# Kernel optimization log

Measured on AMD Instinct MI355X. Metric: run time of the kernel, lower is better.

## Reference

```python
import jax, jax.numpy as jnp
import numpy as np

NBINS = 256
STRENGTH = 100.0
C, H, W = 64, 512, 512


def setup_inputs() -> dict:
    key = jax.random.key(0)
    k1, k2, k3, k4 = jax.random.split(key, 4)
    inp = jax.random.uniform(k1, (1, C, H, W), dtype=jnp.float32)
    tgt = jax.random.uniform(k2, (1, C, H, W), dtype=jnp.float32)
    maskI = jax.random.randint(k3, (1, 1, H, W), 0, 2).astype(jnp.int32)
    maskJ = jax.random.randint(k4, (1, 1, H, W), 0, 2).astype(jnp.int32)
    return {"input": inp, "target": tgt, "maskI": maskI, "maskJ": maskJ}


def _hist_remap(I, J, mI, mJ):
    # I, J: [c, HW] float; mI, mJ: [HW] {0,1} float
    c, hw = I.shape
    nI = mI.sum()
    nJ = mJ.sum()
    big = jnp.float32(1e30)
    # per-channel min/max of masked target values (J[mJ].view(c, nJ).min/max)
    minJ = jnp.min(jnp.where(mJ > 0, J, big), axis=1)   # [c]
    maxJ = jnp.max(jnp.where(mJ > 0, J, -big), axis=1)  # [c]
    step = (maxJ - minJ) / NBINS                          # [c]
    # masked per-channel histogram of target (cu.histogram), scaled by nI/nJ
    binJ = jnp.clip(jnp.floor((J - minJ[:, None]) / jnp.maximum(step[:, None], 1e-12)),
                    0, NBINS - 1).astype(jnp.int32)
    seg = binJ + jnp.arange(c, dtype=jnp.int32)[:, None] * NBINS
    hisJ = jax.ops.segment_sum(jnp.broadcast_to(mJ, (c, hw)).reshape(-1),
                               seg.reshape(-1), num_segments=c * NBINS).reshape(c, NBINS)
    hisJ = hisJ * (nI / nJ)
    cumJ = jnp.cumsum(hisJ, axis=1)                       # [c, nbins]
    # mask input; unmasked pixels -> -1 so they sort to the front (msk_sub trick)
    _I = I * mI - (1.0 - mI)                              # [c, HW]
    idxI = jnp.argsort(_I, axis=1)                        # ascending sort order
    # 1-indexed rank among the nI masked pixels (unmasked ranks <= 0, ignored later)
    rank = jnp.arange(hw, dtype=jnp.float32) - (hw - nI) + 1.0  # [HW]

    def per_ch(cum, his, r, mn, st):
        # CDF inverse: smallest bin b with cum[b] >= rank (cu.hist_remap2)
        b = jnp.clip(jnp.searchsorted(cum, r, side='left'), 0, NBINS - 1)
        lo = cum[b] - his[b]
        ratio = jnp.clip((r - lo) / jnp.maximum(his[b], 1e-12), 0.0, 1.0)
        return mn + (b.astype(jnp.float32) + ratio) * st

    vals = jax.vmap(per_ch)(cumJ, hisJ, jnp.broadcast_to(rank, (c, hw)), minJ, step)  # [c, HW]
    # scatter remapped sorted values back to original pixel positions
    R_sorted = jax.vmap(lambda idx, v: jnp.zeros(hw, dtype=v.dtype).at[idx].set(v))(idxI, vals)
    R = jnp.where(mI > 0, R_sorted, I)
    return R


def reference(input, target, maskI, maskJ):
    _, c, h, w = input.shape
    hw = h * w
    I = input[0].reshape(c, hw)
    J = target[0].reshape(c, hw)
    mI = maskI[0, 0].reshape(hw).astype(jnp.float32)
    mJ = maskJ[0, 0].reshape(hw).astype(jnp.float32)
    R = _hist_remap(I, J, mI, mJ)
    # F.mse_loss(I, R) * strength
    loss = jnp.mean((I - R) ** 2) * STRENGTH
    return loss
```

## Files before the change

### kernel.cpp

```cpp
#include <hip/hip_runtime.h>


#define CN    64
#define HWN   262144
#define NB    256
#define NBUK  8192
#define NBLK  16
#define BPIX  (HWN/NBLK)
#define PT    512
#define XB    64
#define QBUK  (NBUK/4)
#define FXS2  268435456.0f
#define FXSI2 (1.0/268435456.0)

__global__ __launch_bounds__(256) void k_bits(
    const int* __restrict__ mI, const int* __restrict__ mJ,
    unsigned char* __restrict__ bI, unsigned char* __restrict__ bJ)
{
  const int t = blockIdx.x*256 + threadIdx.x;
  const int4* a = (const int4*)mI + 2*t;
  int4 x0 = a[0], x1 = a[1];
  unsigned b = (unsigned)((x0.x>0) | ((x0.y>0)<<1) | ((x0.z>0)<<2) | ((x0.w>0)<<3)
             | ((x1.x>0)<<4) | ((x1.y>0)<<5) | ((x1.z>0)<<6) | ((x1.w>0)<<7));
  const int4* c = (const int4*)mJ + 2*t;
  int4 y0 = c[0], y1 = c[1];
  unsigned d = (unsigned)((y0.x>0) | ((y0.y>0)<<1) | ((y0.z>0)<<2) | ((y0.w>0)<<3)
             | ((y1.x>0)<<4) | ((y1.y>0)<<5) | ((y1.z>0)<<6) | ((y1.w>0)<<7));
  bI[t] = (unsigned char)b;
  bJ[t] = (unsigned char)d;
}

__global__ __launch_bounds__(PT, 4) void k_pass1(
    const float* __restrict__ I, const float* __restrict__ J,
    const unsigned* __restrict__ bI, const unsigned* __restrict__ bJ,
    unsigned* __restrict__ pc, unsigned* __restrict__ qtot,
    unsigned* __restrict__ mnp, unsigned* __restrict__ mxp,
    unsigned* __restrict__ cp, double* __restrict__ qp)
{
  const int c = blockIdx.y, q = blockIdx.x, tid = threadIdx.x;
  const int bid = c*NBLK + q;
  const int wid = tid >> 6, lane = tid & 63;
  __shared__ unsigned buk[NBUK];
  __shared__ unsigned smbI[BPIX/32], smbJ[BPIX/32];
  __shared__ unsigned sred[PT];
  __shared__ double   dred[PT/64];
  __shared__ unsigned umn[PT/64], umx[PT/64], uci[PT/64], ucj[PT/64];
  for(int i = tid; i < NBUK; i += PT) buk[i] = 0u;
  smbI[tid] = bI[q*(BPIX/32) + tid];
  smbJ[tid] = bJ[q*(BPIX/32) + tid];
  __syncthreads();

  const float4* Ic = (const float4*)(I + (size_t)c*HWN + (size_t)q*BPIX);
  const float4* Jc = (const float4*)(J + (size_t)c*HWN + (size_t)q*BPIX);

  float qacc = 0.0f;
  unsigned ci = 0, cj = 0;
  unsigned mn = 0x7F800000u, mx = 0u;
  const int nsh = (tid & 7) * 4;

  float4 pi[2], pj[2];
  pi[0] = Ic[tid]; pj[0] = Jc[tid];
  #pragma unroll
  for(int g = 0; g < 8; g++){
    const int cur = g & 1, nxt = cur ^ 1;
    if(g < 7){ pi[nxt] = Ic[(g+1)*PT + tid]; pj[nxt] = Jc[(g+1)*PT + tid]; }
    const unsigned bitsI = (smbI[g*64 + (tid>>3)] >> nsh) & 0xFu;
    const unsigned bitsJ = (smbJ[g*64 + (tid>>3)] >> nsh) & 0xFu;
    float4 vi4 = pi[cur], vj4 = pj[cur];
    float vv[4] = {vi4.x, vi4.y, vi4.z, vi4.w};
    #pragma unroll
    for(int e = 0; e < 4; e++){
      if(bitsI & (1u << e)){
        float v = vv[e];
        int k = (int)(v * (float)NBUK);
        if(k > NBUK-1) k = NBUK-1;
        float dv = v - ((float)k + 0.5f) * (1.0f/(float)NBUK);
        int fx = (int)rintf(dv * FXS2);
        atomicAdd(&buk[k], ((unsigned)fx << 12) + 1u);
        qacc += dv*dv;
        ci++;
      }
    }
    if(bitsJ & 1u){unsigned u=__float_as_uint(vj4.x); mn=min(mn,u); mx=max(mx,u); cj++;}
    if(bitsJ & 2u){unsigned u=__float_as_uint(vj4.y); mn=min(mn,u); mx=max(mx,u); cj++;}
    if(bitsJ & 4u){unsigned u=__float_as_uint(vj4.z); mn=min(mn,u); mx=max(mx,u); cj++;}
    if(bitsJ & 8u){unsigned u=__float_as_uint(vj4.w); mn=min(mn,u); mx=max(mx,u); cj++;}
  }
  __syncthreads();
  { unsigned* pcb = pc + (size_t)bid * NBUK;
    for(int i = tid; i < NBUK; i += PT) pcb[i] = buk[i]; }

  { unsigned csum = 0;
    #pragma unroll
    for(int j = 0; j < 16; j++) csum += buk[tid*16 + j] & 0xFFFu;
    sred[tid] = csum; __syncthreads();
    for(int s = 64; s > 0; s >>= 1){
      if((tid & 127) < s) sred[tid] += sred[tid + s];
      __syncthreads();
    }
    if((tid & 127) == 0) qtot[bid*4 + (tid >> 7)] = sred[tid];
  }

  double qd = (double)qacc;
  for(int o = 32; o > 0; o >>= 1){
    qd += __shfl_down(qd, o, 64);
    mn  = min(mn, (unsigned)__shfl_down(mn, o, 64));
    mx  = max(mx, (unsigned)__shfl_down(mx, o, 64));
    ci += __shfl_down(ci, o, 64);
    cj += __shfl_down(cj, o, 64);
  }
  if(lane == 0){ dred[wid]=qd; umn[wid]=mn; umx[wid]=mx; uci[wid]=ci; ucj[wid]=cj; }
  __syncthreads();
  if(tid == 0){
    double t = 0.0; unsigned amn=0x7F800000u, amx=0u, aci=0, acj=0;
    for(int w = 0; w < PT/64; w++){
      t += dred[w];
      amn = min(amn, umn[w]); amx = max(amx, umx[w]);
      aci += uci[w]; acj += ucj[w];
    }
    qp[bid] = t;
    mnp[bid] = amn; mxp[bid] = amx;
    if(c == 0){ cp[2*q] = aci; cp[2*q+1] = acj; }
  }
}

__global__ __launch_bounds__(256) void k_histJ(
    const float* __restrict__ J, const unsigned* __restrict__ bJ,
    const unsigned* __restrict__ mnp, const unsigned* __restrict__ mxp,
    unsigned* __restrict__ hisPart, double* __restrict__ lossacc,
    unsigned* __restrict__ donecnt)
{
  const int c = blockIdx.y, xb = blockIdx.x, tid = threadIdx.x;
  if(c == 0 && xb == 0 && tid == 0){ *lossacc = 0.0; *donecnt = 0u; }
  unsigned mnu = 0x7F800000u, mxu = 0u;
  #pragma unroll
  for(int qi = 0; qi < NBLK; qi++){
    mnu = min(mnu, mnp[c*NBLK + qi]);
    mxu = max(mxu, mxp[c*NBLK + qi]);
  }
  float mnv = __uint_as_float(mnu);
  float den = fmaxf((__uint_as_float(mxu) - mnv) / (float)NB, 1e-12f);
  const int SLICE = HWN/XB;
  __shared__ unsigned h[NB];
  __shared__ unsigned smb[SLICE/32];
  h[tid] = 0u;
  if(tid < SLICE/32) smb[tid] = bJ[xb*(SLICE/32) + tid];
  __syncthreads();
  const float4* Jc = (const float4*)(J + (size_t)c*HWN + (size_t)xb*SLICE);
  const int nsh = (tid & 7) * 4;
  #pragma unroll
  for(int it = 0; it < SLICE/1024; ++it){
    int idx = it*256 + tid;
    float4 v4 = Jc[idx];
    const unsigned bits = (smb[it*32 + (tid>>3)] >> nsh) & 0xFu;
    float vv[4] = {v4.x,v4.y,v4.z,v4.w};
    #pragma unroll
    for(int e = 0; e < 4; e++){
      if(bits & (1u << e)){
        float bf = floorf((vv[e] - mnv) / den);
        bf = fminf(fmaxf(bf, 0.0f), 255.0f);
        atomicAdd(&h[(int)bf], 1u);
      }
    }
  }
  __syncthreads();
  hisPart[((size_t)c*XB + xb)*NB + tid] = h[tid];
}

__global__ __launch_bounds__(1024) void k_closs(
    const unsigned* __restrict__ pc, const unsigned* __restrict__ qtot,
    const unsigned* __restrict__ hisPart,
    const unsigned* __restrict__ mnp, const unsigned* __restrict__ mxp,
    const unsigned* __restrict__ cp, const double* __restrict__ qp,
    double* __restrict__ lossacc, unsigned* __restrict__ donecnt,
    float* __restrict__ out)
{
  const int c = blockIdx.x >> 2, qt = blockIdx.x & 3, tid = threadIdx.x;
  const int wid = tid >> 6, lane = tid & 63;
  __shared__ float cs[NB], hs[NB];
  __shared__ unsigned hsum[NB];
  __shared__ unsigned qsh[NBLK*4];
  __shared__ unsigned wsum[16];
  __shared__ double red[16];
  __shared__ float sh_mn, sh_st;
  __shared__ unsigned sh_base;

  if(tid < NB){
    unsigned hr = 0u;
    for(int xb = 0; xb < XB; xb++) hr += hisPart[((size_t)c*XB + xb)*NB + tid];
    hsum[tid] = hr;
  } else if(tid < NB + NBLK*4){
    int k = tid - NB;
    qsh[k] = qtot[(c*NBLK + (k >> 2))*4 + (k & 3)];
  }
  __syncthreads();
  if(tid == 0){
    unsigned ciw = 0, cjw = 0;
    for(int qi = 0; qi < NBLK; qi++){ ciw += cp[2*qi]; cjw += cp[2*qi+1]; }
    float ratio = (float)ciw / (float)cjw;
    float cum = 0.0f;
    for(int b = 0; b < NB; b++){
      float hh = (float)hsum[b] * ratio;
      hs[b] = hh;
      cum += hh;
      cs[b] = cum;
    }
    unsigned mnu = 0x7F800000u, mxu = 0u;
    for(int qi = 0; qi < NBLK; qi++){ mnu = min(mnu, mnp[c*NBLK+qi]); mxu = max(mxu, mxp[c*NBLK+qi]); }
    sh_mn = __uint_as_float(mnu);
    sh_st = (__uint_as_float(mxu) - sh_mn) / (float)NB;
    unsigned base = 0;
    for(int s = 0; s < NBLK; s++)
      for(int q2 = 0; q2 < qt; q2++) base += qsh[s*4 + q2];
    sh_base = base;
  }
  __syncthreads();

  unsigned  kk[2] = {0,0};
  long long ss[2] = {0,0};
  for(int sl = 0; sl < NBLK; sl++){
    const uint2* pcb = (const uint2*)(pc + (size_t)(c*NBLK + sl)*NBUK + qt*QBUK) + tid;
    uint2 w = *pcb;
    kk[0] += w.x & 0xFFFu;  ss[0] += (int)w.x >> 12;
    kk[1] += w.y & 0xFFFu;  ss[1] += (int)w.y >> 12;
  }
  unsigned run = kk[0] + kk[1];
  unsigned v = run;
  for(int o = 1; o < 64; o <<= 1){
    unsigned t = __shfl_up(v, o, 64);
    if(lane >= o) v += t;
  }
  if(lane == 63) wsum[wid] = v;
  __syncthreads();
  unsigned wbase = 0;
  for(int w = 0; w < wid; w++) wbase += wsum[w];
  unsigned texcl = sh_base + wbase + (v - run);

  float  mnvf = sh_mn, stepf = sh_st;
  double mnvd = (double)mnvf, stepd = (double)stepf;

  float rf0 = (float)(texcl + 1u);
  int lo = 0, hi = NB;
  while(lo < hi){ int mid = (lo + hi) >> 1; if(cs[mid] < rf0) lo = mid + 1; else hi = mid; }
  int bin = (lo > NB-1) ? NB-1 : lo;

  double acc = 0.0;
  unsigned r = texcl;
  #pragma unroll
  for(int j = 0; j < 2; j++){
    unsigned k = kk[j];
    if(k == 0) continue;
    unsigned ra = r + 1u, rb = r + k; r = rb;
    double sval = 0.0;
    while(ra <= rb){
      while(bin < NB-1 && cs[bin] < (float)ra) bin++;
      float csb = cs[bin], hsb = hs[bin];
      unsigned re = (bin == NB-1) ? rb : min(rb, (unsigned)floorf(csb));
      double lovd = (double)csb - (double)hsb;
      double den2 = fmax((double)hsb, 1e-12);
      double ra_d = (double)ra, re_d = (double)re, nn = (double)(re - ra + 1u);
      double rta = (ra_d - lovd)/den2, rtb = (re_d - lovd)/den2;
      if(hsb > 0.0f && rta >= 0.0 && rtb <= 1.0){
        double sumr = 0.5*(ra_d + re_d)*nn;
        sval += nn*(mnvd + (double)bin*stepd) + stepd*(sumr - nn*lovd)/den2;
      } else {
        for(unsigned rr = ra; rr <= re; rr++){
          float rf = (float)rr;
          float lov = csb - hsb;
          float rt = (rf - lov) / fmaxf(hsb, 1e-12f);
          rt = fminf(fmaxf(rt, 0.0f), 1.0f);
          sval += (double)(mnvf + ((float)bin + rt)*stepf);
        }
      }
      ra = re + 1u;
    }
    double kb   = (double)k;
    double cb   = ((double)(qt*QBUK + tid*2 + j) + 0.5) * (1.0/(double)NBUK);
    double vbar = sval/kb - cb;
    double S    = (double)ss[j] * FXSI2;
    acc += kb*vbar*vbar - 2.0*vbar*S;
  }
  if(qt == 0 && tid == 0){
    double qsum = 0.0;
    for(int qi = 0; qi < NBLK; qi++) qsum += qp[c*NBLK + qi];
    acc += qsum;
  }
  for(int o = 32; o > 0; o >>= 1) acc += __shfl_down(acc, o, 64);
  if(lane == 0) red[wid] = acc;
  __syncthreads();
  if(tid == 0){
    double t = 0.0;
    for(int w = 0; w < 16; w++) t += red[w];
    atomicAdd(lossacc, t);
    __threadfence();
    unsigned old = atomicAdd(donecnt, 1u);
    if(old == (unsigned)(CN*4 - 1)){
      double tot = atomicAdd(lossacc, 0.0);
      out[0] = (float)(tot * (100.0 / (double)((size_t)CN * HWN)));
    }
  }
}

extern "C" void kernel_launch(void* const* d_in, const int* in_sizes, int n_in,
                              void* d_out, int out_size, void* d_ws, size_t ws_size,
                              hipStream_t stream){
  const float* I  = (const float*)d_in[0];
  const float* J  = (const float*)d_in[1];
  const int*   mI = (const int*)d_in[2];
  const int*   mJ = (const int*)d_in[3];
  float* out = (float*)d_out;

  char* base = (char*)d_ws;
  size_t pcB = (size_t)CN * NBLK * NBUK * sizeof(unsigned);
  size_t hpB = (size_t)CN * XB * NB * sizeof(unsigned);
  size_t qtB = (size_t)CN * NBLK * 4 * sizeof(unsigned);
  unsigned* pc      = (unsigned*)base;
  unsigned* hisPart = (unsigned*)(base + pcB);
  unsigned* qtot    = (unsigned*)(base + pcB + hpB);
  char* p = base + pcB + hpB + qtB;
  double*   qp      = (double*)p;   p += (size_t)CN*NBLK*sizeof(double);
  double*   lossacc = (double*)p;   p += sizeof(double);
  unsigned* mnp     = (unsigned*)p; p += (size_t)CN*NBLK*sizeof(unsigned);
  unsigned* mxp     = (unsigned*)p; p += (size_t)CN*NBLK*sizeof(unsigned);
  unsigned* cp      = (unsigned*)p; p += 2*NBLK*sizeof(unsigned);
  unsigned* donecnt = (unsigned*)p; p += sizeof(unsigned);
  size_t off = (size_t)(p - base); off = (off + 15) & ~(size_t)15;
  unsigned char* bIb = (unsigned char*)(base + off);
  unsigned char* bJb = bIb + HWN/8;

  k_bits<<<HWN/(8*256), 256, 0, stream>>>(mI, mJ, bIb, bJb);
  k_pass1<<<dim3(NBLK, CN), PT, 0, stream>>>(I, J, (const unsigned*)bIb,
                                             (const unsigned*)bJb, pc, qtot,
                                             mnp, mxp, cp, qp);
  k_histJ<<<dim3(XB, CN), 256, 0, stream>>>(J, (const unsigned*)bJb, mnp, mxp,
                                            hisPart, lossacc, donecnt);
  k_closs<<<CN*4, 1024, 0, stream>>>(pc, qtot, hisPart, mnp, mxp, cp, qp,
                                     lossacc, donecnt, out);
}
```

Measured before the change: 189.0 us.

## Front-load all pass1/histJ loads and reshape histJ grid to fewer, larger blocks

k_pass1 now issues all eight float4 loads of I and J, plus the mask words, up front instead of double-buffering them, and its launch bound drops from 4 to 2 blocks per SM to leave room for the extra registers. k_histJ moves from 64 slices of 256 threads to 16 slices of 512 threads, each thread loading all eight vectors at once. Fewer partial histograms are written, and k_closs now spreads the per-bin partial sums across all 1024 threads instead of 256. The goal is more memory-level parallelism and less partial-reduction work, at the cost of higher register pressure and lower occupancy.

```diff
diff --git a/kernel.cpp b/kernel.cpp
--- a/kernel.cpp
+++ b/kernel.cpp
@@ -8,7 +8,8 @@
 #define NBLK  16
 #define BPIX  (HWN/NBLK)
 #define PT    512
-#define XB    64
+#define XB    16
+#define JSL   (HWN/XB)
 #define QBUK  (NBUK/4)
 #define FXS2  268435456.0f
 #define FXSI2 (1.0/268435456.0)
@@ -30,7 +31,31 @@
   bJ[t] = (unsigned char)d;
 }
 
-__global__ __launch_bounds__(PT, 4) void k_pass1(
+__device__ __forceinline__ void px_i(float v, float& qacc, unsigned& ci,
+                                     unsigned* buk){
+  int k = (int)(v * (float)NBUK);
+  if(k > NBUK-1) k = NBUK-1;
+  float dv = v - ((float)k + 0.5f) * (1.0f/(float)NBUK);
+  int fx = (int)rintf(dv * FXS2);
+  atomicAdd(&buk[k], ((unsigned)fx << 12) + 1u);
+  qacc += dv*dv;
+  ci++;
+}
+
+__device__ __forceinline__ void grp_p1(float4 vi4, float4 vj4,
+    unsigned bitsI, unsigned bitsJ, float& qacc, unsigned& ci, unsigned& cj,
+    unsigned& mn, unsigned& mx, unsigned* buk){
+  if(bitsI & 1u) px_i(vi4.x, qacc, ci, buk);
+  if(bitsI & 2u) px_i(vi4.y, qacc, ci, buk);
+  if(bitsI & 4u) px_i(vi4.z, qacc, ci, buk);
+  if(bitsI & 8u) px_i(vi4.w, qacc, ci, buk);
+  if(bitsJ & 1u){unsigned u=__float_as_uint(vj4.x); mn=min(mn,u); mx=max(mx,u); cj++;}
+  if(bitsJ & 2u){unsigned u=__float_as_uint(vj4.y); mn=min(mn,u); mx=max(mx,u); cj++;}
+  if(bitsJ & 4u){unsigned u=__float_as_uint(vj4.z); mn=min(mn,u); mx=max(mx,u); cj++;}
+  if(bitsJ & 8u){unsigned u=__float_as_uint(vj4.w); mn=min(mn,u); mx=max(mx,u); cj++;}
+}
+
+__global__ __launch_bounds__(PT, 2) void k_pass1(
     const float* __restrict__ I, const float* __restrict__ J,
     const unsigned* __restrict__ bI, const unsigned* __restrict__ bJ,
     unsigned* __restrict__ pc, unsigned* __restrict__ qtot,
@@ -57,35 +82,26 @@
   unsigned ci = 0, cj = 0;
   unsigned mn = 0x7F800000u, mx = 0u;
   const int nsh = (tid & 7) * 4;
-
-  float4 pi[2], pj[2];
-  pi[0] = Ic[tid]; pj[0] = Jc[tid];
-  #pragma unroll
-  for(int g = 0; g < 8; g++){
-    const int cur = g & 1, nxt = cur ^ 1;
-    if(g < 7){ pi[nxt] = Ic[(g+1)*PT + tid]; pj[nxt] = Jc[(g+1)*PT + tid]; }
-    const unsigned bitsI = (smbI[g*64 + (tid>>3)] >> nsh) & 0xFu;
-    const unsigned bitsJ = (smbJ[g*64 + (tid>>3)] >> nsh) & 0xFu;
-    float4 vi4 = pi[cur], vj4 = pj[cur];
-    float vv[4] = {vi4.x, vi4.y, vi4.z, vi4.w};
-    #pragma unroll
-    for(int e = 0; e < 4; e++){
-      if(bitsI & (1u << e)){
-        float v = vv[e];
-        int k = (int)(v * (float)NBUK);
-        if(k > NBUK-1) k = NBUK-1;
-        float dv = v - ((float)k + 0.5f) * (1.0f/(float)NBUK);
-        int fx = (int)rintf(dv * FXS2);
-        atomicAdd(&buk[k], ((unsigned)fx << 12) + 1u);
-        qacc += dv*dv;
-        ci++;
-      }
-    }
-    if(bitsJ & 1u){unsigned u=__float_as_uint(vj4.x); mn=min(mn,u); mx=max(mx,u); cj++;}
-    if(bitsJ & 2u){unsigned u=__float_as_uint(vj4.y); mn=min(mn,u); mx=max(mx,u); cj++;}
-    if(bitsJ & 4u){unsigned u=__float_as_uint(vj4.z); mn=min(mn,u); mx=max(mx,u); cj++;}
-    if(bitsJ & 8u){unsigned u=__float_as_uint(vj4.w); mn=min(mn,u); mx=max(mx,u); cj++;}
-  }
+  const int bw  = tid >> 3;
+
+  float4 i0 = Ic[0*PT+tid], i1 = Ic[1*PT+tid], i2 = Ic[2*PT+tid], i3 = Ic[3*PT+tid];
+  float4 i4 = Ic[4*PT+tid], i5 = Ic[5*PT+tid], i6 = Ic[6*PT+tid], i7 = Ic[7*PT+tid];
+  float4 j0 = Jc[0*PT+tid], j1 = Jc[1*PT+tid], j2 = Jc[2*PT+tid], j3 = Jc[3*PT+tid];
+  float4 j4 = Jc[4*PT+tid], j5 = Jc[5*PT+tid], j6 = Jc[6*PT+tid], j7 = Jc[7*PT+tid];
+  unsigned wi0=smbI[0*64+bw], wi1=smbI[1*64+bw], wi2=smbI[2*64+bw], wi3=smbI[3*64+bw];
+  unsigned wi4=smbI[4*64+bw], wi5=smbI[5*64+bw], wi6=smbI[6*64+bw], wi7=smbI[7*64+bw];
+  unsigned wj0=smbJ[0*64+bw], wj1=smbJ[1*64+bw], wj2=smbJ[2*64+bw], wj3=smbJ[3*64+bw];
+  unsigned wj4=smbJ[4*64+bw], wj5=smbJ[5*64+bw], wj6=smbJ[6*64+bw], wj7=smbJ[7*64+bw];
+
+  grp_p1(i0, j0, (wi0>>nsh)&0xFu, (wj0>>nsh)&0xFu, qacc, ci, cj, mn, mx, buk);
+  grp_p1(i1, j1, (wi1>>nsh)&0xFu, (wj1>>nsh)&0xFu, qacc, ci, cj, mn, mx, buk);
+  grp_p1(i2, j2, (wi2>>nsh)&0xFu, (wj2>>nsh)&0xFu, qacc, ci, cj, mn, mx, buk);
+  grp_p1(i3, j3, (wi3>>nsh)&0xFu, (wj3>>nsh)&0xFu, qacc, ci, cj, mn, mx, buk);
+  grp_p1(i4, j4, (wi4>>nsh)&0xFu, (wj4>>nsh)&0xFu, qacc, ci, cj, mn, mx, buk);
+  grp_p1(i5, j5, (wi5>>nsh)&0xFu, (wj5>>nsh)&0xFu, qacc, ci, cj, mn, mx, buk);
+  grp_p1(i6, j6, (wi6>>nsh)&0xFu, (wj6>>nsh)&0xFu, qacc, ci, cj, mn, mx, buk);
+  grp_p1(i7, j7, (wi7>>nsh)&0xFu, (wj7>>nsh)&0xFu, qacc, ci, cj, mn, mx, buk);
+
   __syncthreads();
   { unsigned* pcb = pc + (size_t)bid * NBUK;
     for(int i = tid; i < NBUK; i += PT) pcb[i] = buk[i]; }
@@ -124,7 +140,31 @@
   }
 }
 
-__global__ __launch_bounds__(256) void k_histJ(
+__device__ __forceinline__ void grp_hj(float4 v4, unsigned bits,
+    float mnv, float den, unsigned* h){
+  if(bits & 1u){
+    float bf = floorf((v4.x - mnv) / den);
+    bf = fminf(fmaxf(bf, 0.0f), 255.0f);
+    atomicAdd(&h[(int)bf], 1u);
+  }
+  if(bits & 2u){
+    float bf = floorf((v4.y - mnv) / den);
+    bf = fminf(fmaxf(bf, 0.0f), 255.0f);
+    atomicAdd(&h[(int)bf], 1u);
+  }
+  if(bits & 4u){
+    float bf = floorf((v4.z - mnv) / den);
+    bf = fminf(fmaxf(bf, 0.0f), 255.0f);
+    atomicAdd(&h[(int)bf], 1u);
+  }
+  if(bits & 8u){
+    float bf = floorf((v4.w - mnv) / den);
+    bf = fminf(fmaxf(bf, 0.0f), 255.0f);
+    atomicAdd(&h[(int)bf], 1u);
+  }
+}
+
+__global__ __launch_bounds__(512, 2) void k_histJ(
     const float* __restrict__ J, const unsigned* __restrict__ bJ,
     const unsigned* __restrict__ mnp, const unsigned* __restrict__ mxp,
     unsigned* __restrict__ hisPart, double* __restrict__ lossacc,
@@ -140,31 +180,28 @@
   }
   float mnv = __uint_as_float(mnu);
   float den = fmaxf((__uint_as_float(mxu) - mnv) / (float)NB, 1e-12f);
-  const int SLICE = HWN/XB;
   __shared__ unsigned h[NB];
-  __shared__ unsigned smb[SLICE/32];
-  h[tid] = 0u;
-  if(tid < SLICE/32) smb[tid] = bJ[xb*(SLICE/32) + tid];
-  __syncthreads();
-  const float4* Jc = (const float4*)(J + (size_t)c*HWN + (size_t)xb*SLICE);
+  __shared__ unsigned smb[JSL/32];
+  if(tid < NB) h[tid] = 0u;
+  smb[tid] = bJ[xb*(JSL/32) + tid];
+  __syncthreads();
+  const float4* Jc = (const float4*)(J + (size_t)c*HWN + (size_t)xb*JSL);
   const int nsh = (tid & 7) * 4;
-  #pragma unroll
-  for(int it = 0; it < SLICE/1024; ++it){
-    int idx = it*256 + tid;
-    float4 v4 = Jc[idx];
-    const unsigned bits = (smb[it*32 + (tid>>3)] >> nsh) & 0xFu;
-    float vv[4] = {v4.x,v4.y,v4.z,v4.w};
-    #pragma unroll
-    for(int e = 0; e < 4; e++){
-      if(bits & (1u << e)){
-        float bf = floorf((vv[e] - mnv) / den);
-        bf = fminf(fmaxf(bf, 0.0f), 255.0f);
-        atomicAdd(&h[(int)bf], 1u);
-      }
-    }
-  }
-  __syncthreads();
-  hisPart[((size_t)c*XB + xb)*NB + tid] = h[tid];
+  const int bw  = tid >> 3;
+  float4 v0 = Jc[0*512+tid], v1 = Jc[1*512+tid], v2 = Jc[2*512+tid], v3 = Jc[3*512+tid];
+  float4 v4 = Jc[4*512+tid], v5 = Jc[5*512+tid], v6 = Jc[6*512+tid], v7 = Jc[7*512+tid];
+  unsigned w0=smb[0*64+bw], w1=smb[1*64+bw], w2=smb[2*64+bw], w3=smb[3*64+bw];
+  unsigned w4=smb[4*64+bw], w5=smb[5*64+bw], w6=smb[6*64+bw], w7=smb[7*64+bw];
+  grp_hj(v0, (w0>>nsh)&0xFu, mnv, den, h);
+  grp_hj(v1, (w1>>nsh)&0xFu, mnv, den, h);
+  grp_hj(v2, (w2>>nsh)&0xFu, mnv, den, h);
+  grp_hj(v3, (w3>>nsh)&0xFu, mnv, den, h);
+  grp_hj(v4, (w4>>nsh)&0xFu, mnv, den, h);
+  grp_hj(v5, (w5>>nsh)&0xFu, mnv, den, h);
+  grp_hj(v6, (w6>>nsh)&0xFu, mnv, den, h);
+  grp_hj(v7, (w7>>nsh)&0xFu, mnv, den, h);
+  __syncthreads();
+  if(tid < NB) hisPart[((size_t)c*XB + xb)*NB + tid] = h[tid];
 }
 
 __global__ __launch_bounds__(1024) void k_closs(
@@ -179,20 +216,23 @@
   const int wid = tid >> 6, lane = tid & 63;
   __shared__ float cs[NB], hs[NB];
   __shared__ unsigned hsum[NB];
+  __shared__ unsigned ph[4][NB];
   __shared__ unsigned qsh[NBLK*4];
   __shared__ unsigned wsum[16];
   __shared__ double red[16];
   __shared__ float sh_mn, sh_st;
   __shared__ unsigned sh_base;
 
-  if(tid < NB){
+  { const int part = tid >> 8, bin = tid & 255;
     unsigned hr = 0u;
-    for(int xb = 0; xb < XB; xb++) hr += hisPart[((size_t)c*XB + xb)*NB + tid];
-    hsum[tid] = hr;
-  } else if(tid < NB + NBLK*4){
-    int k = tid - NB;
-    qsh[k] = qtot[(c*NBLK + (k >> 2))*4 + (k & 3)];
-  }
+    #pragma unroll
+    for(int x = 0; x < 4; x++)
+      hr += hisPart[((size_t)c*XB + (part*4 + x))*NB + bin];
+    ph[part][bin] = hr; }
+  if(tid < NBLK*4)
+    qsh[tid] = qtot[(c*NBLK + (tid >> 2))*4 + (tid & 3)];
+  __syncthreads();
+  if(tid < NB) hsum[tid] = ph[0][tid] + ph[1][tid] + ph[2][tid] + ph[3][tid];
   __syncthreads();
   if(tid == 0){
     unsigned ciw = 0, cjw = 0;
@@ -332,7 +372,7 @@
   k_pass1<<<dim3(NBLK, CN), PT, 0, stream>>>(I, J, (const unsigned*)bIb,
                                              (const unsigned*)bJb, pc, qtot,
                                              mnp, mxp, cp, qp);
-  k_histJ<<<dim3(XB, CN), 256, 0, stream>>>(J, (const unsigned*)bJb, mnp, mxp,
+  k_histJ<<<dim3(XB, CN), 512, 0, stream>>>(J, (const unsigned*)bJb, mnp, mxp,
                                             hisPart, lossacc, donecnt);
   k_closs<<<CN*4, 1024, 0, stream>>>(pc, qtot, hisPart, mnp, mxp, cp, qp,
                                      lossacc, donecnt, out);
```

New measurement: 188.1 us. No clear change (-0.5%).

## Fuse pass1, target histogram and loss kernels with per-channel spin barriers

Applied to the files above, without the earlier changes.

Merges the three kernels after the mask-bit pass into one persistent kernel with 4 blocks of 1024 threads per channel. The blocks of a channel meet at global atomic spin barriers before the target histogram and before the loss stage, and the per-block histograms are merged through global atomics. This removes two kernel launches and the separate reread of partial results, and the J slice may still be in cache when the histogram pass reads it. The cost is far fewer blocks (256), which limits parallelism, and the spin barriers assume every block of a channel is resident at the same time.

```diff
diff --git a/kernel.cpp b/kernel.cpp
--- a/kernel.cpp
+++ b/kernel.cpp
@@ -5,19 +5,26 @@
 #define HWN   262144
 #define NB    256
 #define NBUK  8192
-#define NBLK  16
-#define BPIX  (HWN/NBLK)
-#define PT    512
-#define XB    64
+#define NSL   4
+#define QPIX  (HWN/NSL)
+#define FT    1024
 #define QBUK  (NBUK/4)
 #define FXS2  268435456.0f
 #define FXSI2 (1.0/268435456.0)
 
 __global__ __launch_bounds__(256) void k_bits(
     const int* __restrict__ mI, const int* __restrict__ mJ,
-    unsigned char* __restrict__ bI, unsigned char* __restrict__ bJ)
+    unsigned char* __restrict__ bI, unsigned char* __restrict__ bJ,
+    unsigned* __restrict__ ghist, unsigned* __restrict__ syncbuf,
+    double* __restrict__ lossacc, unsigned* __restrict__ donecnt)
 {
   const int t = blockIdx.x*256 + threadIdx.x;
+  if(blockIdx.x < 64){
+    ghist[blockIdx.x*NB + threadIdx.x] = 0u;
+  } else if(blockIdx.x == 64){
+    for(int i = threadIdx.x; i < 2048; i += 256) syncbuf[i] = 0u;
+    if(threadIdx.x == 0){ *lossacc = 0.0; *donecnt = 0u; }
+  }
   const int4* a = (const int4*)mI + 2*t;
   int4 x0 = a[0], x1 = a[1];
   unsigned b = (unsigned)((x0.x>0) | ((x0.y>0)<<1) | ((x0.z>0)<<2) | ((x0.w>0)<<3)
@@ -30,75 +37,91 @@
   bJ[t] = (unsigned char)d;
 }
 
-__global__ __launch_bounds__(PT, 4) void k_pass1(
+__device__ __forceinline__ void px_i(float v, float& qacc, unsigned* buk){
+  int k = (int)(v * (float)NBUK);
+  if(k > NBUK-1) k = NBUK-1;
+  float dv = v - ((float)k + 0.5f) * (1.0f/(float)NBUK);
+  int fx = (int)rintf(dv * FXS2);
+  atomicAdd(&buk[k], ((unsigned)fx << 12) + 1u);
+  qacc += dv*dv;
+}
+
+__device__ __forceinline__ void grp_p1(float4 vi, float4 vj,
+    unsigned bI4, unsigned bJ4, float& qacc, unsigned& mn, unsigned& mx,
+    unsigned* buk){
+  if(bI4 & 1u) px_i(vi.x, qacc, buk);
+  if(bI4 & 2u) px_i(vi.y, qacc, buk);
+  if(bI4 & 4u) px_i(vi.z, qacc, buk);
+  if(bI4 & 8u) px_i(vi.w, qacc, buk);
+  if(bJ4 & 1u){unsigned u=__float_as_uint(vj.x); mn=min(mn,u); mx=max(mx,u);}
+  if(bJ4 & 2u){unsigned u=__float_as_uint(vj.y); mn=min(mn,u); mx=max(mx,u);}
+  if(bJ4 & 4u){unsigned u=__float_as_uint(vj.z); mn=min(mn,u); mx=max(mx,u);}
+  if(bJ4 & 8u){unsigned u=__float_as_uint(vj.w); mn=min(mn,u); mx=max(mx,u);}
+}
+
+__global__ __launch_bounds__(FT, 4) void k_fused(
     const float* __restrict__ I, const float* __restrict__ J,
     const unsigned* __restrict__ bI, const unsigned* __restrict__ bJ,
-    unsigned* __restrict__ pc, unsigned* __restrict__ qtot,
-    unsigned* __restrict__ mnp, unsigned* __restrict__ mxp,
-    unsigned* __restrict__ cp, double* __restrict__ qp)
+    unsigned* pc, unsigned* qtot, unsigned* mnp, unsigned* mxp,
+    unsigned* cip, unsigned* cjp, double* qp, unsigned* ghist,
+    unsigned* sync1, unsigned* sync2,
+    double* lossacc, unsigned* donecnt, float* out)
 {
-  const int c = blockIdx.y, q = blockIdx.x, tid = threadIdx.x;
-  const int bid = c*NBLK + q;
+  const int c = blockIdx.y, qt = blockIdx.x, tid = threadIdx.x;
+  const int bid4 = c*NSL + qt;
   const int wid = tid >> 6, lane = tid & 63;
   __shared__ unsigned buk[NBUK];
-  __shared__ unsigned smbI[BPIX/32], smbJ[BPIX/32];
-  __shared__ unsigned sred[PT];
-  __shared__ double   dred[PT/64];
-  __shared__ unsigned umn[PT/64], umx[PT/64], uci[PT/64], ucj[PT/64];
-  for(int i = tid; i < NBUK; i += PT) buk[i] = 0u;
-  smbI[tid] = bI[q*(BPIX/32) + tid];
-  smbJ[tid] = bJ[q*(BPIX/32) + tid];
-  __syncthreads();
-
-  const float4* Ic = (const float4*)(I + (size_t)c*HWN + (size_t)q*BPIX);
-  const float4* Jc = (const float4*)(J + (size_t)c*HWN + (size_t)q*BPIX);
-
+  __shared__ unsigned smbI[QPIX/32], smbJ[QPIX/32];
+  __shared__ unsigned sred[FT];
+  __shared__ unsigned h[NB], hsum[NB];
+  __shared__ float cs[NB], hs[NB];
+  __shared__ double dred[FT/64];
+  __shared__ unsigned umn[FT/64], umx[FT/64], uci[FT/64], ucj[FT/64];
+  __shared__ unsigned qsh[16], wsum[FT/64];
+  __shared__ double red[FT/64];
+  __shared__ float sh_mn, sh_den, sh_st;
+  __shared__ unsigned sh_base;
+
+  const int qb = qt*(QPIX/32);
+  unsigned s0 = bI[qb + tid], s1 = bI[qb + tid + 1024];
+  unsigned t0 = bJ[qb + tid], t1 = bJ[qb + tid + 1024];
+  smbI[tid] = s0; smbI[tid+1024] = s1;
+  smbJ[tid] = t0; smbJ[tid+1024] = t1;
+  unsigned ci = __popc(s0) + __popc(s1);
+  unsigned cj = __popc(t0) + __popc(t1);
+  #pragma unroll
+  for(int i = 0; i < 8; i++) buk[i*FT + tid] = 0u;
+  __syncthreads();
+
+  const float4* Ic = (const float4*)(I + (size_t)c*HWN + (size_t)qt*QPIX);
+  const float4* Jc = (const float4*)(J + (size_t)c*HWN + (size_t)qt*QPIX);
   float qacc = 0.0f;
-  unsigned ci = 0, cj = 0;
   unsigned mn = 0x7F800000u, mx = 0u;
   const int nsh = (tid & 7) * 4;
-
-  float4 pi[2], pj[2];
-  pi[0] = Ic[tid]; pj[0] = Jc[tid];
+  const int bw  = tid >> 3;
   #pragma unroll
-  for(int g = 0; g < 8; g++){
-    const int cur = g & 1, nxt = cur ^ 1;
-    if(g < 7){ pi[nxt] = Ic[(g+1)*PT + tid]; pj[nxt] = Jc[(g+1)*PT + tid]; }
-    const unsigned bitsI = (smbI[g*64 + (tid>>3)] >> nsh) & 0xFu;
-    const unsigned bitsJ = (smbJ[g*64 + (tid>>3)] >> nsh) & 0xFu;
-    float4 vi4 = pi[cur], vj4 = pj[cur];
-    float vv[4] = {vi4.x, vi4.y, vi4.z, vi4.w};
+  for(int g = 0; g < 16; g++){
+    float4 vi = Ic[g*FT + tid];
+    float4 vj = Jc[g*FT + tid];
+    unsigned bI4 = (smbI[g*128 + bw] >> nsh) & 0xFu;
+    unsigned bJ4 = (smbJ[g*128 + bw] >> nsh) & 0xFu;
+    grp_p1(vi, vj, bI4, bJ4, qacc, mn, mx, buk);
+  }
+  __syncthreads();
+
+  { unsigned* pcb = pc + (size_t)bid4 * NBUK;
     #pragma unroll
-    for(int e = 0; e < 4; e++){
-      if(bitsI & (1u << e)){
-        float v = vv[e];
-        int k = (int)(v * (float)NBUK);
-        if(k > NBUK-1) k = NBUK-1;
-        float dv = v - ((float)k + 0.5f) * (1.0f/(float)NBUK);
-        int fx = (int)rintf(dv * FXS2);
-        atomicAdd(&buk[k], ((unsigned)fx << 12) + 1u);
-        qacc += dv*dv;
-        ci++;
-      }
-    }
-    if(bitsJ & 1u){unsigned u=__float_as_uint(vj4.x); mn=min(mn,u); mx=max(mx,u); cj++;}
-    if(bitsJ & 2u){unsigned u=__float_as_uint(vj4.y); mn=min(mn,u); mx=max(mx,u); cj++;}
-    if(bitsJ & 4u){unsigned u=__float_as_uint(vj4.z); mn=min(mn,u); mx=max(mx,u); cj++;}
-    if(bitsJ & 8u){unsigned u=__float_as_uint(vj4.w); mn=min(mn,u); mx=max(mx,u); cj++;}
-  }
-  __syncthreads();
-  { unsigned* pcb = pc + (size_t)bid * NBUK;
-    for(int i = tid; i < NBUK; i += PT) pcb[i] = buk[i]; }
+    for(int i = 0; i < 8; i++) pcb[i*FT + tid] = buk[i*FT + tid]; }
 
   { unsigned csum = 0;
     #pragma unroll
-    for(int j = 0; j < 16; j++) csum += buk[tid*16 + j] & 0xFFFu;
+    for(int j = 0; j < 8; j++) csum += buk[tid*8 + j] & 0xFFFu;
     sred[tid] = csum; __syncthreads();
-    for(int s = 64; s > 0; s >>= 1){
-      if((tid & 127) < s) sred[tid] += sred[tid + s];
+    for(int s = 128; s > 0; s >>= 1){
+      if((tid & 255) < s) sred[tid] += sred[tid + s];
       __syncthreads();
     }
-    if((tid & 127) == 0) qtot[bid*4 + (tid >> 7)] = sred[tid];
+    if((tid & 255) == 0) qtot[bid4*4 + (tid >> 8)] = sred[tid];
   }
 
   double qd = (double)qacc;
@@ -113,90 +136,76 @@
   __syncthreads();
   if(tid == 0){
     double t = 0.0; unsigned amn=0x7F800000u, amx=0u, aci=0, acj=0;
-    for(int w = 0; w < PT/64; w++){
+    for(int w = 0; w < FT/64; w++){
       t += dred[w];
       amn = min(amn, umn[w]); amx = max(amx, umx[w]);
       aci += uci[w]; acj += ucj[w];
     }
-    qp[bid] = t;
-    mnp[bid] = amn; mxp[bid] = amx;
-    if(c == 0){ cp[2*q] = aci; cp[2*q+1] = acj; }
-  }
-}
-
-__global__ __launch_bounds__(256) void k_histJ(
-    const float* __restrict__ J, const unsigned* __restrict__ bJ,
-    const unsigned* __restrict__ mnp, const unsigned* __restrict__ mxp,
-    unsigned* __restrict__ hisPart, double* __restrict__ lossacc,
-    unsigned* __restrict__ donecnt)
-{
-  const int c = blockIdx.y, xb = blockIdx.x, tid = threadIdx.x;
-  if(c == 0 && xb == 0 && tid == 0){ *lossacc = 0.0; *donecnt = 0u; }
-  unsigned mnu = 0x7F800000u, mxu = 0u;
-  #pragma unroll
-  for(int qi = 0; qi < NBLK; qi++){
-    mnu = min(mnu, mnp[c*NBLK + qi]);
-    mxu = max(mxu, mxp[c*NBLK + qi]);
-  }
-  float mnv = __uint_as_float(mnu);
-  float den = fmaxf((__uint_as_float(mxu) - mnv) / (float)NB, 1e-12f);
-  const int SLICE = HWN/XB;
-  __shared__ unsigned h[NB];
-  __shared__ unsigned smb[SLICE/32];
-  h[tid] = 0u;
-  if(tid < SLICE/32) smb[tid] = bJ[xb*(SLICE/32) + tid];
-  __syncthreads();
-  const float4* Jc = (const float4*)(J + (size_t)c*HWN + (size_t)xb*SLICE);
-  const int nsh = (tid & 7) * 4;
-  #pragma unroll
-  for(int it = 0; it < SLICE/1024; ++it){
-    int idx = it*256 + tid;
-    float4 v4 = Jc[idx];
-    const unsigned bits = (smb[it*32 + (tid>>3)] >> nsh) & 0xFu;
-    float vv[4] = {v4.x,v4.y,v4.z,v4.w};
+    qp[bid4] = t; mnp[bid4] = amn; mxp[bid4] = amx;
+    cip[bid4] = aci; cjp[bid4] = acj;
+  }
+
+  __syncthreads();
+  __threadfence();
+  if(tid == 0){
+    atomicAdd(&sync1[c*16], 1u);
+    while(__hip_atomic_load(&sync1[c*16], __ATOMIC_ACQUIRE,
+                            __HIP_MEMORY_SCOPE_AGENT) < 4u)
+      __builtin_amdgcn_s_sleep(2);
+  }
+  __syncthreads();
+
+  if(tid < NB) h[tid] = 0u;
+  if(tid == 0){
+    unsigned amn = 0x7F800000u, amx = 0u;
+    for(int i = 0; i < NSL; i++){
+      amn = min(amn, atomicOr(&mnp[c*NSL + i], 0u));
+      amx = max(amx, atomicOr(&mxp[c*NSL + i], 0u));
+    }
+    float mnv = __uint_as_float(amn);
+    float rng = __uint_as_float(amx) - mnv;
+    sh_mn = mnv;
+    sh_den = fmaxf(rng / (float)NB, 1e-12f);
+    sh_st  = rng / (float)NB;
+  }
+  __syncthreads();
+  { const float mnv = sh_mn, den = sh_den;
     #pragma unroll
-    for(int e = 0; e < 4; e++){
-      if(bits & (1u << e)){
-        float bf = floorf((vv[e] - mnv) / den);
-        bf = fminf(fmaxf(bf, 0.0f), 255.0f);
-        atomicAdd(&h[(int)bf], 1u);
-      }
-    }
-  }
-  __syncthreads();
-  hisPart[((size_t)c*XB + xb)*NB + tid] = h[tid];
-}
-
-__global__ __launch_bounds__(1024) void k_closs(
-    const unsigned* __restrict__ pc, const unsigned* __restrict__ qtot,
-    const unsigned* __restrict__ hisPart,
-    const unsigned* __restrict__ mnp, const unsigned* __restrict__ mxp,
-    const unsigned* __restrict__ cp, const double* __restrict__ qp,
-    double* __restrict__ lossacc, unsigned* __restrict__ donecnt,
-    float* __restrict__ out)
-{
-  const int c = blockIdx.x >> 2, qt = blockIdx.x & 3, tid = threadIdx.x;
-  const int wid = tid >> 6, lane = tid & 63;
-  __shared__ float cs[NB], hs[NB];
-  __shared__ unsigned hsum[NB];
-  __shared__ unsigned qsh[NBLK*4];
-  __shared__ unsigned wsum[16];
-  __shared__ double red[16];
-  __shared__ float sh_mn, sh_st;
-  __shared__ unsigned sh_base;
-
-  if(tid < NB){
-    unsigned hr = 0u;
-    for(int xb = 0; xb < XB; xb++) hr += hisPart[((size_t)c*XB + xb)*NB + tid];
-    hsum[tid] = hr;
-  } else if(tid < NB + NBLK*4){
-    int k = tid - NB;
-    qsh[k] = qtot[(c*NBLK + (k >> 2))*4 + (k & 3)];
-  }
+    for(int g = 0; g < 16; g++){
+      float4 v = Jc[g*FT + tid];
+      unsigned b4 = (smbJ[g*128 + bw] >> nsh) & 0xFu;
+      if(b4 & 1u){ float bf = floorf((v.x - mnv)/den);
+        bf = fminf(fmaxf(bf,0.0f),255.0f); atomicAdd(&h[(int)bf],1u); }
+      if(b4 & 2u){ float bf = floorf((v.y - mnv)/den);
+        bf = fminf(fmaxf(bf,0.0f),255.0f); atomicAdd(&h[(int)bf],1u); }
+      if(b4 & 4u){ float bf = floorf((v.z - mnv)/den);
+        bf = fminf(fmaxf(bf,0.0f),255.0f); atomicAdd(&h[(int)bf],1u); }
+      if(b4 & 8u){ float bf = floorf((v.w - mnv)/den);
+        bf = fminf(fmaxf(bf,0.0f),255.0f); atomicAdd(&h[(int)bf],1u); }
+    }
+  }
+  __syncthreads();
+  if(tid < NB) atomicAdd(&ghist[c*NB + tid], h[tid]);
+  __threadfence();
+  if(tid == 0){
+    atomicAdd(&sync2[c*16], 1u);
+    while(__hip_atomic_load(&sync2[c*16], __ATOMIC_ACQUIRE,
+                            __HIP_MEMORY_SCOPE_AGENT) < 4u)
+      __builtin_amdgcn_s_sleep(2);
+  }
+  __syncthreads();
+
+  if(tid < 16)
+    qsh[tid] = atomicOr(&qtot[(c*NSL + (tid>>2))*4 + (tid&3)], 0u);
+  if(tid < NB)
+    hsum[tid] = atomicAdd(&ghist[c*NB + tid], 0u);
   __syncthreads();
   if(tid == 0){
     unsigned ciw = 0, cjw = 0;
-    for(int qi = 0; qi < NBLK; qi++){ ciw += cp[2*qi]; cjw += cp[2*qi+1]; }
+    for(int i = 0; i < NSL; i++){
+      ciw += atomicOr(&cip[c*NSL + i], 0u);
+      cjw += atomicOr(&cjp[c*NSL + i], 0u);
+    }
     float ratio = (float)ciw / (float)cjw;
     float cum = 0.0f;
     for(int b = 0; b < NB; b++){
@@ -205,12 +214,8 @@
       cum += hh;
       cs[b] = cum;
     }
-    unsigned mnu = 0x7F800000u, mxu = 0u;
-    for(int qi = 0; qi < NBLK; qi++){ mnu = min(mnu, mnp[c*NBLK+qi]); mxu = max(mxu, mxp[c*NBLK+qi]); }
-    sh_mn = __uint_as_float(mnu);
-    sh_st = (__uint_as_float(mxu) - sh_mn) / (float)NB;
     unsigned base = 0;
-    for(int s = 0; s < NBLK; s++)
+    for(int s = 0; s < NSL; s++)
       for(int q2 = 0; q2 < qt; q2++) base += qsh[s*4 + q2];
     sh_base = base;
   }
@@ -218,11 +223,13 @@
 
   unsigned  kk[2] = {0,0};
   long long ss[2] = {0,0};
-  for(int sl = 0; sl < NBLK; sl++){
-    const uint2* pcb = (const uint2*)(pc + (size_t)(c*NBLK + sl)*NBUK + qt*QBUK) + tid;
-    uint2 w = *pcb;
-    kk[0] += w.x & 0xFFFu;  ss[0] += (int)w.x >> 12;
-    kk[1] += w.y & 0xFFFu;  ss[1] += (int)w.y >> 12;
+  for(int sl = 0; sl < NSL; sl++){
+    unsigned long long* pcb = (unsigned long long*)
+        (pc + (size_t)(c*NSL + sl)*NBUK + qt*QBUK) + tid;
+    unsigned long long o = atomicAdd(pcb, 0ULL);
+    unsigned wx = (unsigned)o, wy = (unsigned)(o >> 32);
+    kk[0] += wx & 0xFFFu;  ss[0] += (int)wx >> 12;
+    kk[1] += wy & 0xFFFu;  ss[1] += (int)wy >> 12;
   }
   unsigned run = kk[0] + kk[1];
   unsigned v = run;
@@ -282,7 +289,8 @@
   }
   if(qt == 0 && tid == 0){
     double qsum = 0.0;
-    for(int qi = 0; qi < NBLK; qi++) qsum += qp[c*NBLK + qi];
+    for(int qi = 0; qi < NSL; qi++)
+      qsum += atomicAdd(&qp[c*NSL + qi], 0.0);
     acc += qsum;
   }
   for(int o = 32; o > 0; o >>= 1) acc += __shfl_down(acc, o, 64);
@@ -290,11 +298,11 @@
   __syncthreads();
   if(tid == 0){
     double t = 0.0;
-    for(int w = 0; w < 16; w++) t += red[w];
+    for(int w = 0; w < FT/64; w++) t += red[w];
     atomicAdd(lossacc, t);
     __threadfence();
     unsigned old = atomicAdd(donecnt, 1u);
-    if(old == (unsigned)(CN*4 - 1)){
+    if(old == (unsigned)(CN*NSL - 1)){
       double tot = atomicAdd(lossacc, 0.0);
       out[0] = (float)(tot * (100.0 / (double)((size_t)CN * HWN)));
     }
@@ -311,29 +319,29 @@
   float* out = (float*)d_out;
 
   char* base = (char*)d_ws;
-  size_t pcB = (size_t)CN * NBLK * NBUK * sizeof(unsigned);
-  size_t hpB = (size_t)CN * XB * NB * sizeof(unsigned);
-  size_t qtB = (size_t)CN * NBLK * 4 * sizeof(unsigned);
+  size_t pcB = (size_t)CN * NSL * NBUK * sizeof(unsigned);
   unsigned* pc      = (unsigned*)base;
-  unsigned* hisPart = (unsigned*)(base + pcB);
-  unsigned* qtot    = (unsigned*)(base + pcB + hpB);
-  char* p = base + pcB + hpB + qtB;
-  double*   qp      = (double*)p;   p += (size_t)CN*NBLK*sizeof(double);
+  char* p = base + pcB;
+  double*   qp      = (double*)p;   p += (size_t)CN*NSL*sizeof(double);
   double*   lossacc = (double*)p;   p += sizeof(double);
-  unsigned* mnp     = (unsigned*)p; p += (size_t)CN*NBLK*sizeof(unsigned);
-  unsigned* mxp     = (unsigned*)p; p += (size_t)CN*NBLK*sizeof(unsigned);
-  unsigned* cp      = (unsigned*)p; p += 2*NBLK*sizeof(unsigned);
+  unsigned* qtot    = (unsigned*)p; p += (size_t)CN*NSL*4*sizeof(unsigned);
+  unsigned* mnp     = (unsigned*)p; p += (size_t)CN*NSL*sizeof(unsigned);
+  unsigned* mxp     = (unsigned*)p; p += (size_t)CN*NSL*sizeof(unsigned);
+  unsigned* cip     = (unsigned*)p; p += (size_t)CN*NSL*sizeof(unsigned);
+  unsigned* cjp     = (unsigned*)p; p += (size_t)CN*NSL*sizeof(unsigned);
+  unsigned* ghist   = (unsigned*)p; p += (size_t)CN*NB*sizeof(unsigned);
+  unsigned* syncbuf = (unsigned*)p; p += 2048*sizeof(unsigned);
   unsigned* donecnt = (unsigned*)p; p += sizeof(unsigned);
   size_t off = (size_t)(p - base); off = (off + 15) & ~(size_t)15;
   unsigned char* bIb = (unsigned char*)(base + off);
   unsigned char* bJb = bIb + HWN/8;
-
-  k_bits<<<HWN/(8*256), 256, 0, stream>>>(mI, mJ, bIb, bJb);
-  k_pass1<<<dim3(NBLK, CN), PT, 0, stream>>>(I, J, (const unsigned*)bIb,
-                                             (const unsigned*)bJb, pc, qtot,
-                                             mnp, mxp, cp, qp);
-  k_histJ<<<dim3(XB, CN), 256, 0, stream>>>(J, (const unsigned*)bJb, mnp, mxp,
-                                            hisPart, lossacc, donecnt);
-  k_closs<<<CN*4, 1024, 0, stream>>>(pc, qtot, hisPart, mnp, mxp, cp, qp,
-                                     lossacc, donecnt, out);
-}
+  unsigned* sync1 = syncbuf;
+  unsigned* sync2 = syncbuf + 1024;
+
+  k_bits<<<HWN/(8*256), 256, 0, stream>>>(mI, mJ, bIb, bJb, ghist, syncbuf,
+                                          lossacc, donecnt);
+  k_fused<<<dim3(NSL, CN), FT, 0, stream>>>(I, J, (const unsigned*)bIb,
+                                            (const unsigned*)bJb, pc, qtot,
+                                            mnp, mxp, cip, cjp, qp, ghist,
+                                            sync1, sync2, lossacc, donecnt, out);
+}
```

After: 307.0 us. +62.4%, slower.
